# Performance work log

Measured on AMD Instinct MI355X. Metric: run time of the kernel, lower is better.

Reference implementation:

```python
import jax, jax.numpy as jnp
import numpy as np

WIN = 9           # local NCC window per axis
PAD = WIN // 2    # 'same' zero padding, matches F.conv3d(padding=4)
DN = ('NCDHW', 'OIDHW', 'NCDHW')


def box_sum(x):
    """9x9x9 local sum via separable 1D ones-filter convs (zero padding).
    Mathematically identical to conv3d with a 9^3 ones kernel."""
    for ax in range(3):
        kshape = [1, 1, 1, 1, 1]
        kshape[2 + ax] = WIN
        k = jnp.ones(kshape, x.dtype)
        pad = [(0, 0)] * 3
        pad[ax] = (PAD, PAD)
        x = jax.lax.conv_general_dilated(x, k, (1, 1, 1), pad, dimension_numbers=DN)
    return x


def nas_ncc(I, J):
    win_size = WIN ** 3
    I_sum = box_sum(I)
    J_sum = box_sum(J)
    I2_sum = box_sum(I * I)
    J2_sum = box_sum(J * J)
    IJ_sum = box_sum(I * J)
    u_I = I_sum / win_size
    u_J = J_sum / win_size
    cross = IJ_sum - u_J * I_sum - u_I * J_sum + u_I * u_J * win_size
    I_var = I2_sum - 2.0 * u_I * I_sum + u_I * u_I * win_size
    J_var = J2_sum - 2.0 * u_J * J_sum + u_J * u_J * win_size
    cc = cross * cross / (I_var * J_var + 1e-5)
    return -jnp.mean(cc)


def gradient_loss_l2(s):
    # finite differences along D, H, W of flow [B, 3, D, H, W]; l2 penalty
    dy = jnp.square(s[:, :, 1:, :, :] - s[:, :, :-1, :, :])
    dx = jnp.square(s[:, :, :, 1:, :] - s[:, :, :, :-1, :])
    dz = jnp.square(s[:, :, :, :, 1:] - s[:, :, :, :, :-1])
    return (jnp.mean(dx) + jnp.mean(dy) + jnp.mean(dz)) / 3.0


def setup_inputs() -> dict:
    key = jax.random.key(0)
    k1, k2, k3, k4 = jax.random.split(key, 4)
    shp = (1, 1, 160, 160, 160)
    return {
        'y': jax.random.normal(k1, shp, dtype=jnp.float32),
        'tgt': jax.random.normal(k2, shp, dtype=jnp.float32),
        'src': jax.random.normal(k3, shp, dtype=jnp.float32),
        'flow': jax.random.normal(k4, (1, 3, 160, 160, 160), dtype=jnp.float32),
    }


def reference(y, tgt, src, flow):
    hyper_1 = 10.0
    hyper_2 = 15.0
    ncc = nas_ncc(tgt, y)
    grad = gradient_loss_l2(flow)
    loss = hyper_1 * ncc + hyper_2 * grad
    return (loss, ncc, grad)
```

## Files before the change

kernel.cpp:

```cpp
#include <hip/hip_runtime.h>

#define DIM 160
#define PLANE 25600
#define NVOX 4096000
constexpr float INV_WS = 1.0f / 729.0f;

#define TW 32
#define TH 16
#define DC 16
#define HW 40
#define HH 24
#define PSTR 41
#define WSTR 33

#define NCC_WAVES 4000
#define GRAD_WAVES 4096

__global__ __launch_bounds__(512)
void ncc_fused_kernel(const float* __restrict__ I, const float* __restrict__ J,
                      double* __restrict__ part) {
    __shared__ float prod[5][HH * PSTR];
    __shared__ float wsum[5][HH * WSTR];

    const int tid = threadIdx.x;
    const int w0 = blockIdx.x * TW;
    const int h0 = blockIdx.y * TH;
    const int d0 = blockIdx.z * DC;
    const int wi = tid & 31;
    const int hi = tid >> 5;

    const int p0 = tid;
    const int r0 = p0 / HW, c0 = p0 - r0 * HW;
    const int p1 = tid + 512;
    const int r1 = p1 / HW, c1 = p1 - r1 * HW;
    const int gr0 = h0 - 4 + r0, gc0 = w0 - 4 + c0;
    const int gr1 = h0 - 4 + r1, gc1 = w0 - 4 + c1;
    const bool v0 = (gr0 >= 0 && gr0 < DIM && gc0 >= 0 && gc0 < DIM);
    const bool v1 = (p1 < HH * HW) && (gr1 >= 0 && gr1 < DIM && gc1 >= 0 && gc1 < DIM);
    const int off0 = gr0 * DIM + gc0;
    const int off1 = gr1 * DIM + gc1;

    const int tf   = tid / 96;
    const int trm  = tid - tf * 96;
    const int tr   = trm >> 2;
    const int tseg = (trm & 3) * 8;

    float S[5][9];
    #pragma unroll
    for (int f = 0; f < 5; ++f)
        #pragma unroll
        for (int s = 0; s < 9; ++s) S[f][s] = 0.f;
    float R[5] = {0.f, 0.f, 0.f, 0.f, 0.f};
    float local = 0.f;

    for (int k0 = 0; k0 < DC + 8; k0 += 9) {
        #pragma unroll
        for (int j = 0; j < 9; ++j) {
            const int k = k0 + j;
            if (k < DC + 8) {
                const int ds = d0 - 4 + k;
                if (ds >= 0 && ds < DIM) {
                    const int sb = ds * PLANE;
                    {
                        float a = 0.f, b = 0.f;
                        if (v0) { a = I[sb + off0]; b = J[sb + off0]; }
                        const int o = r0 * PSTR + c0;
                        prod[0][o] = a; prod[1][o] = b;
                        prod[2][o] = a * a; prod[3][o] = b * b; prod[4][o] = a * b;
                        if (p1 < HH * HW) {
                            float a1 = 0.f, b1 = 0.f;
                            if (v1) { a1 = I[sb + off1]; b1 = J[sb + off1]; }
                            const int o1 = r1 * PSTR + c1;
                            prod[0][o1] = a1; prod[1][o1] = b1;
                            prod[2][o1] = a1 * a1; prod[3][o1] = b1 * b1; prod[4][o1] = a1 * b1;
                        }
                    }
                    __syncthreads();
                    if (tid < 480) {
                        float c[16];
                        #pragma unroll
                        for (int q = 0; q < 16; ++q) c[q] = prod[tf][tr * PSTR + tseg + q];
                        float s = c[0] + c[1] + c[2] + c[3] + c[4] + c[5] + c[6] + c[7] + c[8];
                        wsum[tf][tr * WSTR + tseg] = s;
                        #pragma unroll
                        for (int q = 1; q < 8; ++q) {
                            s += c[q + 8] - c[q - 1];
                            wsum[tf][tr * WSTR + tseg + q] = s;
                        }
                    }
                    __syncthreads();
                    #pragma unroll
                    for (int f = 0; f < 5; ++f) {
                        float P = 0.f;
                        #pragma unroll
                        for (int q = 0; q < 9; ++q) P += wsum[f][(hi + q) * WSTR + wi];
                        R[f] += P - S[f][j];
                        S[f][j] = P;
                    }
                } else {
                    #pragma unroll
                    for (int f = 0; f < 5; ++f) { R[f] -= S[f][j]; S[f][j] = 0.f; }
                }
                if (k >= 8) {
                    float cross = R[4] - R[0] * R[1] * INV_WS;
                    float Iv    = R[2] - R[0] * R[0] * INV_WS;
                    float Jv    = R[3] - R[1] * R[1] * INV_WS;
                    local += cross * cross / (Iv * Jv + 1e-5f);
                }
            }
        }
    }

    for (int off = 32; off; off >>= 1) local += __shfl_down(local, off);
    if ((tid & 63) == 0) {
        int wave = ((blockIdx.z * gridDim.y + blockIdx.y) * gridDim.x + blockIdx.x) * 8
                 + (tid >> 6);
        part[wave] = (double)local;
    }
}

__global__ void grad_kernel(const float* __restrict__ s, double* __restrict__ part) {
    const int Q = NVOX / 4;
    const float4* s4 = (const float4*)s;
    float local = 0.f;
    for (int q = blockIdx.x * 256 + threadIdx.x; q < Q; q += gridDim.x * 256) {
        int w4   = q % (DIM / 4);
        int rest = q / (DIM / 4);
        int h = rest % DIM;
        int d = rest / DIM;
        #pragma unroll
        for (int c = 0; c < 3; ++c) {
            const int qi = c * Q + q;
            float4 v = s4[qi];
            float t;
            t = v.y - v.x; local += t * t;
            t = v.z - v.y; local += t * t;
            t = v.w - v.z; local += t * t;
            if (w4 < DIM / 4 - 1) {
                float nx = s[c * NVOX + q * 4 + 4];
                t = nx - v.w; local += t * t;
            }
            if (h < DIM - 1) {
                float4 vh = s4[qi + DIM / 4];
                t = vh.x - v.x; local += t * t;
                t = vh.y - v.y; local += t * t;
                t = vh.z - v.z; local += t * t;
                t = vh.w - v.w; local += t * t;
            }
            if (d < DIM - 1) {
                float4 vd = s4[qi + PLANE / 4];
                t = vd.x - v.x; local += t * t;
                t = vd.y - v.y; local += t * t;
                t = vd.z - v.z; local += t * t;
                t = vd.w - v.w; local += t * t;
            }
        }
    }
    for (int off = 32; off; off >>= 1) local += __shfl_down(local, off);
    if ((threadIdx.x & 63) == 0) {
        int wave = blockIdx.x * 4 + (threadIdx.x >> 6);
        part[NCC_WAVES + wave] = (double)local;
    }
}

__global__ void final_kernel(const double* __restrict__ part, float* __restrict__ out) {
    __shared__ double s_n[4], s_g[4];
    double n = 0.0, g = 0.0;
    for (int i = threadIdx.x; i < NCC_WAVES; i += 256) n += part[i];
    for (int i = threadIdx.x; i < GRAD_WAVES; i += 256) g += part[NCC_WAVES + i];
    for (int off = 32; off; off >>= 1) {
        n += __shfl_down(n, off);
        g += __shfl_down(g, off);
    }
    if ((threadIdx.x & 63) == 0) {
        s_n[threadIdx.x >> 6] = n;
        s_g[threadIdx.x >> 6] = g;
    }
    __syncthreads();
    if (threadIdx.x == 0) {
        double ncc_sum  = s_n[0] + s_n[1] + s_n[2] + s_n[3];
        double grad_sum = s_g[0] + s_g[1] + s_g[2] + s_g[3];
        double ncc  = -(ncc_sum / 4096000.0);
        double grad = grad_sum / 36633600.0;
        double loss = 10.0 * ncc + 15.0 * grad;
        out[0] = (float)loss;
        out[1] = (float)ncc;
        out[2] = (float)grad;
    }
}

extern "C" void kernel_launch(void* const* d_in, const int* in_sizes, int n_in,
                              void* d_out, int out_size, void* d_ws, size_t ws_size,
                              hipStream_t stream) {
    const float* y    = (const float*)d_in[0];
    const float* tgt  = (const float*)d_in[1];
    const float* flow = (const float*)d_in[3];
    float* out = (float*)d_out;
    double* part = (double*)d_ws;

    dim3 g1(DIM / TW, DIM / TH, DIM / DC);
    ncc_fused_kernel<<<g1, 512, 0, stream>>>(tgt, y, part);
    grad_kernel<<<1024, 256, 0, stream>>>(flow, part);
    final_kernel<<<1, 256, 0, stream>>>(part, out);
}
```

Baseline: 180.3 us.

## Add sliding-window H pass in NCC and depth-marching grad kernel

The NCC kernel now does the H-direction box sum with a running-window pass into a new shared buffer, so each thread reads one value instead of summing nine rows per field. The W pass gives each thread 16 outputs instead of 8, using fewer threads. This adds an extra __syncthreads per slice and leaves many threads idle during the two passes. The grad kernel is reorganised so each thread walks 40 depth slices and reuses the previous slice's float4 instead of reloading it; this uses a 300-block 3D grid instead of a 1024-block grid-stride loop.

```diff
diff --git a/kernel.cpp b/kernel.cpp
--- a/kernel.cpp
+++ b/kernel.cpp
@@ -14,13 +14,14 @@
 #define WSTR 33
 
 #define NCC_WAVES 4000
-#define GRAD_WAVES 4096
+#define GRAD_WAVES 1200
 
 __global__ __launch_bounds__(512)
 void ncc_fused_kernel(const float* __restrict__ I, const float* __restrict__ J,
                       double* __restrict__ part) {
     __shared__ float prod[5][HH * PSTR];
     __shared__ float wsum[5][HH * WSTR];
+    __shared__ float hcol[5][TH * WSTR];
 
     const int tid = threadIdx.x;
     const int w0 = blockIdx.x * TW;
@@ -29,8 +30,7 @@
     const int wi = tid & 31;
     const int hi = tid >> 5;
 
-    const int p0 = tid;
-    const int r0 = p0 / HW, c0 = p0 - r0 * HW;
+    const int r0 = tid / HW, c0 = tid - r0 * HW;
     const int p1 = tid + 512;
     const int r1 = p1 / HW, c1 = p1 - r1 * HW;
     const int gr0 = h0 - 4 + r0, gc0 = w0 - 4 + c0;
@@ -40,10 +40,13 @@
     const int off0 = gr0 * DIM + gc0;
     const int off1 = gr1 * DIM + gc1;
 
-    const int tf   = tid / 96;
-    const int trm  = tid - tf * 96;
-    const int tr   = trm >> 2;
-    const int tseg = (trm & 3) * 8;
+    const int wt_f    = tid / 48;
+    const int wt_rem  = tid - wt_f * 48;
+    const int wt_r    = wt_rem >> 1;
+    const int wt_base = (wt_rem & 1) * 16;
+
+    const int ht_f = tid >> 5;
+    const int ht_w = tid & 31;
 
     float S[5][9];
     #pragma unroll
@@ -76,24 +79,37 @@
                         }
                     }
                     __syncthreads();
-                    if (tid < 480) {
-                        float c[16];
-                        #pragma unroll
-                        for (int q = 0; q < 16; ++q) c[q] = prod[tf][tr * PSTR + tseg + q];
-                        float s = c[0] + c[1] + c[2] + c[3] + c[4] + c[5] + c[6] + c[7] + c[8];
-                        wsum[tf][tr * WSTR + tseg] = s;
-                        #pragma unroll
-                        for (int q = 1; q < 8; ++q) {
+                    if (tid < 240) {
+                        float c[24];
+                        #pragma unroll
+                        for (int q = 0; q < 24; ++q)
+                            c[q] = prod[wt_f][wt_r * PSTR + wt_base + q];
+                        float s = c[0]+c[1]+c[2]+c[3]+c[4]+c[5]+c[6]+c[7]+c[8];
+                        wsum[wt_f][wt_r * WSTR + wt_base] = s;
+                        #pragma unroll
+                        for (int q = 1; q < 16; ++q) {
                             s += c[q + 8] - c[q - 1];
-                            wsum[tf][tr * WSTR + tseg + q] = s;
+                            wsum[wt_f][wt_r * WSTR + wt_base + q] = s;
+                        }
+                    }
+                    __syncthreads();
+                    if (tid < 160) {
+                        float c[24];
+                        #pragma unroll
+                        for (int q = 0; q < 24; ++q)
+                            c[q] = wsum[ht_f][q * WSTR + ht_w];
+                        float s = c[0]+c[1]+c[2]+c[3]+c[4]+c[5]+c[6]+c[7]+c[8];
+                        hcol[ht_f][ht_w] = s;
+                        #pragma unroll
+                        for (int q = 1; q < 16; ++q) {
+                            s += c[q + 8] - c[q - 1];
+                            hcol[ht_f][q * WSTR + ht_w] = s;
                         }
                     }
                     __syncthreads();
                     #pragma unroll
                     for (int f = 0; f < 5; ++f) {
-                        float P = 0.f;
-                        #pragma unroll
-                        for (int q = 0; q < 9; ++q) P += wsum[f][(hi + q) * WSTR + wi];
+                        float P = hcol[f][hi * WSTR + wi];
                         R[f] += P - S[f][j];
                         S[f][j] = P;
                     }
@@ -122,44 +138,46 @@
 __global__ void grad_kernel(const float* __restrict__ s, double* __restrict__ part) {
     const int Q = NVOX / 4;
     const float4* s4 = (const float4*)s;
+    const int w4 = blockIdx.x * 8 + (threadIdx.x & 7);
+    const int h  = blockIdx.y * 32 + (threadIdx.x >> 3);
+    const int c  = blockIdx.z >> 2;
+    const int d0 = (blockIdx.z & 3) * 40;
+    const int qbase = c * Q + h * (DIM / 4) + w4;
+
     float local = 0.f;
-    for (int q = blockIdx.x * 256 + threadIdx.x; q < Q; q += gridDim.x * 256) {
-        int w4   = q % (DIM / 4);
-        int rest = q / (DIM / 4);
-        int h = rest % DIM;
-        int d = rest / DIM;
-        #pragma unroll
-        for (int c = 0; c < 3; ++c) {
-            const int qi = c * Q + q;
-            float4 v = s4[qi];
-            float t;
-            t = v.y - v.x; local += t * t;
-            t = v.z - v.y; local += t * t;
-            t = v.w - v.z; local += t * t;
-            if (w4 < DIM / 4 - 1) {
-                float nx = s[c * NVOX + q * 4 + 4];
-                t = nx - v.w; local += t * t;
-            }
-            if (h < DIM - 1) {
-                float4 vh = s4[qi + DIM / 4];
-                t = vh.x - v.x; local += t * t;
-                t = vh.y - v.y; local += t * t;
-                t = vh.z - v.z; local += t * t;
-                t = vh.w - v.w; local += t * t;
-            }
-            if (d < DIM - 1) {
-                float4 vd = s4[qi + PLANE / 4];
-                t = vd.x - v.x; local += t * t;
-                t = vd.y - v.y; local += t * t;
-                t = vd.z - v.z; local += t * t;
-                t = vd.w - v.w; local += t * t;
-            }
-        }
-    }
+    float4 v = s4[qbase + d0 * (PLANE / 4)];
+    for (int step = 0; step < 40; ++step) {
+        const int d = d0 + step;
+        const int qi = qbase + d * (PLANE / 4);
+        float t;
+        t = v.y - v.x; local += t * t;
+        t = v.z - v.y; local += t * t;
+        t = v.w - v.z; local += t * t;
+        if (w4 < DIM / 4 - 1) {
+            float nx = s[(qi + 1) * 4];
+            t = nx - v.w; local += t * t;
+        }
+        if (h < DIM - 1) {
+            float4 vh = s4[qi + DIM / 4];
+            t = vh.x - v.x; local += t * t;
+            t = vh.y - v.y; local += t * t;
+            t = vh.z - v.z; local += t * t;
+            t = vh.w - v.w; local += t * t;
+        }
+        if (d < DIM - 1) {
+            float4 vn = s4[qi + PLANE / 4];
+            t = vn.x - v.x; local += t * t;
+            t = vn.y - v.y; local += t * t;
+            t = vn.z - v.z; local += t * t;
+            t = vn.w - v.w; local += t * t;
+            v = vn;
+        }
+    }
+
     for (int off = 32; off; off >>= 1) local += __shfl_down(local, off);
     if ((threadIdx.x & 63) == 0) {
-        int wave = blockIdx.x * 4 + (threadIdx.x >> 6);
-        part[NCC_WAVES + wave] = (double)local;
+        int linear = (blockIdx.z * gridDim.y + blockIdx.y) * gridDim.x + blockIdx.x;
+        part[NCC_WAVES + linear * 4 + (threadIdx.x >> 6)] = (double)local;
     }
 }
 
@@ -200,6 +218,7 @@
 
     dim3 g1(DIM / TW, DIM / TH, DIM / DC);
     ncc_fused_kernel<<<g1, 512, 0, stream>>>(tgt, y, part);
-    grad_kernel<<<1024, 256, 0, stream>>>(flow, part);
+    dim3 g2(5, 5, 12);
+    grad_kernel<<<g2, 256, 0, stream>>>(flow, part);
     final_kernel<<<1, 256, 0, stream>>>(part, out);
 }
```

After: 205.4 us. +13.9%, slower.
